# Kernel optimization log

Measured on AMD Instinct MI355X. Metric: run time of the kernel, lower is better.

The kernel has to match this reference:

```python
import jax, jax.numpy as jnp
import numpy as np

B, S, H = 8, 2048, 1024

def setup_inputs() -> dict:
    key = jax.random.key(0)
    k1, k2, k3, k4, k5, k6 = jax.random.split(key, 6)
    scale = 1.0 / np.sqrt(H)
    return {
        "hidden_states": jax.random.normal(k1, (B, S, H), dtype=jnp.float32),
        "key_padding_mask": jax.random.bernoulli(k2, 0.1, (B, S)),  # True = padded key
        "Wq_w": jax.random.normal(k3, (H, H), dtype=jnp.float32) * scale,
        "Wq_b": jax.random.normal(k4, (H,), dtype=jnp.float32) * 0.01,
        "Wk_w": jax.random.normal(k5, (H, H), dtype=jnp.float32) * scale,
        "Wk_b": jax.random.normal(k6, (H,), dtype=jnp.float32) * 0.01,
    }

def reference(hidden_states, key_padding_mask, Wq_w, Wq_b, Wk_w, Wk_b):
    # torch nn.Linear: y = x @ W.T + b
    q = jnp.einsum("bsh,oh->bso", hidden_states, Wq_w) + Wq_b
    k = jnp.einsum("bsh,oh->bso", hidden_states, Wk_w) + Wk_b
    d = q.shape[-1]
    scores = jnp.einsum("bqd,bkd->bqk", q, k) / jnp.sqrt(jnp.asarray(d, q.dtype))
    # scores[mask] -= inf  -> masked key columns become -inf
    scores = jnp.where(key_padding_mask[:, None, :], -jnp.inf, scores)
    attn = jax.nn.softmax(scores, axis=2)  # [B, S, S]
    out = jnp.einsum("bqk,bkd->bqd", attn, hidden_states)  # values = hidden_states (no proj)
    return out
```

## Files before the change

### kernel.cpp

```cpp
#include <hip/hip_runtime.h>
#include <hip/hip_bf16.h>

using bf16 = __hip_bfloat16;

using frag_ab = __attribute__((ext_vector_type(8))) short;
using frag_cd = __attribute__((ext_vector_type(4))) float;

#define TM 128
#define TN 128
#define TK 32

__device__ __forceinline__ unsigned short f2bu(float f) {
    bf16 h = __float2bfloat16(f);
    return *(unsigned short*)&h;
}
__device__ __forceinline__ float bu2f(unsigned short u) {
    unsigned int w = (unsigned int)u << 16;
    return *(float*)&w;
}

__device__ __forceinline__ void st_c(float* p, float v) { *p = v; }
__device__ __forceinline__ void st_c(bf16* p, float v)  { *p = __float2bfloat16(v); }

__device__ __forceinline__ void load16(const bf16* g, bf16* l) {
    __builtin_amdgcn_global_load_lds(
        (const __attribute__((address_space(1))) unsigned int*)g,
        (__attribute__((address_space(3))) unsigned int*)l,
        16, 0, 0);
}

template <typename TC, bool HAS_BIAS, bool MASK>
__global__ __launch_bounds__(512, 2)
void gemm8p(const bf16* __restrict__ A, const bf16* __restrict__ B,
            const float* __restrict__ bias, const int* __restrict__ mask,
            TC* __restrict__ C, int K, int lda, int ldb, int ldc,
            long sA, long sB, long sC, long sM, long sBias, float scale)
{
    __shared__ short lds[65536];

    const int bz = blockIdx.z;
    const bf16* Ab = A + (long)bz * sA;
    const bf16* Bb = B + (long)bz * sB;
    TC* Cb = C + (long)bz * sC;
    const int* maskb = MASK ? (mask + (long)bz * sM) : nullptr;
    const float* biasb = HAS_BIAS ? (bias + (long)bz * sBias) : nullptr;

    const int t    = threadIdx.x;
    const int wid  = t >> 6;
    const int lane = t & 63;
    const int m0 = blockIdx.x * 256;
    const int n0 = blockIdx.y * 256;
    const int wr = wid >> 2;
    const int wc = wid & 3;
    const int lrow = lane & 15;
    const int quad = lane >> 4;

    const int rco   = ((quad + ((lrow >> 1) & 3)) & 3) * 8;
    const int a_off = wr * 4096 + lrow * 32 + rco;
    const int b_off = wc * 2048 + lrow * 32 + rco;

    const int srow = wid * 32 + (lane >> 2);
    const int gk   = (((lane & 3) - (lane >> 3)) & 3) * 8;
    const bf16* srcA0 = Ab + (long)(m0 + srow) * lda + gk;
    const bf16* srcA1 = Ab + (long)(m0 + srow + 16) * lda + gk;
    const bf16* srcB0 = Bb + (long)(n0 + srow) * ldb + gk;
    const bf16* srcB1 = Bb + (long)(n0 + srow + 16) * ldb + gk;
    const int dst0 = wid * 1024 + lane * 8;

    frag_cd acc[8][4] = {};
    frag_ab A0[4], A1[4], B0[4], B1[4];

#define STG(SLOT, PART, K0)                                                     \
    do {                                                                        \
        load16((PART ? srcB0 : srcA0) + (K0),                                   \
               (bf16*)&lds[(SLOT) * 16384 + (PART) * 8192 + dst0]);             \
        load16((PART ? srcB1 : srcA1) + (K0),                                   \
               (bf16*)&lds[(SLOT) * 16384 + (PART) * 8192 + dst0 + 512]);       \
    } while (0)

#define LOADA(DST, SLOT, QM)                                                    \
    do {                                                                        \
        _Pragma("unroll")                                                       \
        for (int i_ = 0; i_ < 4; ++i_)                                          \
            DST[i_] = *(const frag_ab*)&lds[(SLOT) * 16384 + a_off +            \
                                            (QM) * 2048 + i_ * 512];            \
    } while (0)

#define LOADB(DST, SLOT)                                                        \
    do {                                                                        \
        _Pragma("unroll")                                                       \
        for (int j_ = 0; j_ < 4; ++j_)                                          \
            DST[j_] = *(const frag_ab*)&lds[(SLOT) * 16384 + 8192 + b_off +     \
                                            j_ * 512];                          \
    } while (0)

#define MFMA16(AR, BR, QM)                                                      \
    do {                                                                        \
        _Pragma("unroll")                                                       \
        for (int i_ = 0; i_ < 4; ++i_)                                          \
            _Pragma("unroll")                                                   \
            for (int j_ = 0; j_ < 4; ++j_)                                      \
                acc[(QM) * 4 + i_][j_] = __builtin_amdgcn_mfma_f32_16x16x32_bf16( \
                    AR[i_], BR[j_], acc[(QM) * 4 + i_][j_], 0, 0, 0);           \
    } while (0)

#define VMW(N)                                                                  \
    do {                                                                        \
        if ((N) == 6)      asm volatile("s_waitcnt vmcnt(6)" ::: "memory");     \
        else if ((N) == 4) asm volatile("s_waitcnt vmcnt(4)" ::: "memory");     \
        else if ((N) == 0) asm volatile("s_waitcnt vmcnt(0)" ::: "memory");     \
    } while (0)

#define PH(AR, BR, QM, ISSUE, NSLOT, NAR, NBR, NQM, DO_STG, SSLOT, SPART, SK0, VMN) \
    do {                                                                        \
        if ((ISSUE) >= 1) LOADA(NAR, NSLOT, NQM);                               \
        if ((ISSUE) == 2) LOADB(NBR, NSLOT);                                    \
        if (DO_STG) STG(SSLOT, SPART, SK0);                                     \
        asm volatile("" ::: "memory");                                          \
        __builtin_amdgcn_s_setprio(1);                                          \
        MFMA16(AR, BR, QM);                                                     \
        __builtin_amdgcn_s_setprio(0);                                          \
        VMW(VMN);                                                               \
        asm volatile("" ::: "memory");                                          \
        __builtin_amdgcn_s_barrier();                                           \
        asm volatile("" ::: "memory");                                          \
    } while (0)

    STG(0, 0, 0);  STG(0, 1, 0);
    STG(1, 0, 32); STG(1, 1, 32);
    STG(2, 0, 64); STG(2, 1, 64);
    asm volatile("s_waitcnt vmcnt(8)" ::: "memory");
    __builtin_amdgcn_s_barrier();
    asm volatile("" ::: "memory");
    LOADA(A0, 0, 0);
    LOADB(B0, 0);

    const int NI = K >> 7;
    for (int it = 0; it < NI - 1; ++it) {
        const int kb = it << 7;
        PH(A0, B0, 0, 1, 0, A1, B1, 1, 1, 3, 0, kb + 96,   6);
        PH(A1, B0, 1, 2, 1, A0, B1, 0, 1, 3, 1, kb + 96,  -1);
        PH(A0, B1, 0, 1, 1, A1, B0, 1, 1, 0, 0, kb + 128,  6);
        PH(A1, B1, 1, 2, 2, A0, B0, 0, 1, 0, 1, kb + 128, -1);
        PH(A0, B0, 0, 1, 2, A1, B1, 1, 1, 1, 0, kb + 160,  6);
        PH(A1, B0, 1, 2, 3, A0, B1, 0, 1, 1, 1, kb + 160, -1);
        PH(A0, B1, 0, 1, 3, A1, B0, 1, 1, 2, 0, kb + 192,  6);
        PH(A1, B1, 1, 2, 0, A0, B0, 0, 1, 2, 1, kb + 192, -1);
    }
    {
        const int kb = (NI - 1) << 7;
        PH(A0, B0, 0, 1, 0, A1, B1, 1, 1, 3, 0, kb + 96,   6);
        PH(A1, B0, 1, 2, 1, A0, B1, 0, 1, 3, 1, kb + 96,  -1);
        PH(A0, B1, 0, 1, 1, A1, B0, 1, 0, 0, 0, 0,         4);
        PH(A1, B1, 1, 2, 2, A0, B0, 0, 0, 0, 0, 0,        -1);
        PH(A0, B0, 0, 1, 2, A1, B1, 1, 0, 0, 0, 0,         0);
        PH(A1, B0, 1, 2, 3, A0, B1, 0, 0, 0, 0, 0,        -1);
        PH(A0, B1, 0, 1, 3, A1, B0, 1, 0, 0, 0, 0,        -1);
        PH(A1, B1, 1, 0, 0, A0, B0, 0, 0, 0, 0, 0,        -1);
    }
#undef PH
#undef VMW
#undef MFMA16
#undef LOADB
#undef LOADA
#undef STG

#pragma unroll
    for (int j = 0; j < 4; ++j) {
        const int col = n0 + wc * 64 + j * 16 + lrow;
        const float bv = HAS_BIAS ? biasb[col] : 0.0f;
        const bool msk = MASK ? (maskb[col] != 0) : false;
#pragma unroll
        for (int ai = 0; ai < 8; ++ai) {
            const int rbase = m0 + wr * 128 + ai * 16 + quad * 4;
#pragma unroll
            for (int r = 0; r < 4; ++r) {
                float v = acc[ai][j][r] * scale + bv;
                if (MASK && msk) v = -INFINITY;
                st_c(&Cb[(long)(rbase + r) * ldc + col], v);
            }
        }
    }
}

template <typename TC, bool HAS_BIAS, bool MASK>
__global__ __launch_bounds__(256, 4)
void mfma_gemm_nt(const bf16* __restrict__ A, const bf16* __restrict__ B,
                  const float* __restrict__ bias, const int* __restrict__ mask,
                  TC* __restrict__ C, int N, int K, int lda, int ldb, int ldc,
                  long sA, long sB, long sC, long sM, float scale)
{
    __shared__ bf16 As[2][TM][TK];
    __shared__ bf16 Bs[2][TN][TK];

    const int bz = blockIdx.z;
    const bf16* Ab = A + (long)bz * sA;
    const bf16* Bb = B + (long)bz * sB;
    TC* Cb = C + (long)bz * sC;
    const int* maskb = MASK ? (mask + (long)bz * sM) : nullptr;

    const int t  = threadIdx.x;
    const int m0 = blockIdx.x * TM;
    const int n0 = blockIdx.y * TN;

    const int srow = t >> 2;
    const int c    = t & 3;
    const int gco  = (((c - (srow >> 1)) & 3) << 3);
    const int lco  = c << 3;
    const bf16* ga0 = Ab + (long)(m0 + srow) * lda + gco;
    const bf16* ga1 = ga0 + (long)64 * lda;
    const bf16* gb0 = Bb + (long)(n0 + srow) * ldb + gco;
    const bf16* gb1 = gb0 + (long)64 * ldb;

    const int wave = t >> 6;
    const int lane = t & 63;
    const int wm   = (wave & 1) * 64;
    const int wn   = (wave >> 1) * 64;
    const int lrow = lane & 15;
    const int quad = lane >> 4;
    const int rco  = (((quad + (lrow >> 1)) & 3) << 3);

    frag_cd acc[4][4] = {};

#define STAGE(buf)                                         \
    do {                                                   \
        load16(ga0, &As[buf][srow][lco]);                  \
        load16(ga1, &As[buf][srow + 64][lco]);             \
        load16(gb0, &Bs[buf][srow][lco]);                  \
        load16(gb1, &Bs[buf][srow + 64][lco]);             \
        ga0 += TK; ga1 += TK; gb0 += TK; gb1 += TK;        \
    } while (0)

    STAGE(0);
    __syncthreads();

    int cur = 0;
    for (int k0 = 0; k0 < K; k0 += TK) {
        if (k0 + TK < K) STAGE(cur ^ 1);

        frag_ab af[4], bfv[4];
#pragma unroll
        for (int i = 0; i < 4; ++i)
            af[i] = *(const frag_ab*)&As[cur][wm + i * 16 + lrow][rco];
#pragma unroll
        for (int j = 0; j < 4; ++j)
            bfv[j] = *(const frag_ab*)&Bs[cur][wn + j * 16 + lrow][rco];
#pragma unroll
        for (int i = 0; i < 4; ++i)
#pragma unroll
            for (int j = 0; j < 4; ++j)
                acc[i][j] = __builtin_amdgcn_mfma_f32_16x16x32_bf16(
                    af[i], bfv[j], acc[i][j], 0, 0, 0);

        __syncthreads();
        cur ^= 1;
    }
#undef STAGE

#pragma unroll
    for (int j = 0; j < 4; ++j) {
        const int col = n0 + wn + j * 16 + lrow;
        const float bv = HAS_BIAS ? bias[col] : 0.0f;
        const bool msk = MASK ? (maskb[col] != 0) : false;
#pragma unroll
        for (int i = 0; i < 4; ++i) {
            const int rbase = m0 + wm + i * 16 + quad * 4;
#pragma unroll
            for (int r = 0; r < 4; ++r) {
                float v = acc[i][j][r] * scale + bv;
                if (MASK && msk) v = -INFINITY;
                st_c(&Cb[(long)(rbase + r) * ldc + col], v);
            }
        }
    }
}

__global__ __launch_bounds__(256)
void convert_transpose(const float* __restrict__ X, bf16* __restrict__ Xb,
                       bf16* __restrict__ XT, int S, int H)
{
    __shared__ unsigned short tile[64][72];
    const int b = blockIdx.z;
    const float* Xp = X + (long)b * S * H;
    bf16* Xbp = Xb + (long)b * S * H;
    bf16* XTp = XT + (long)b * H * S;
    const int h0 = blockIdx.x * 64, s0 = blockIdx.y * 64;
    const int t = threadIdx.x;
    const int r  = t >> 4;
    const int c4 = (t & 15) * 4;

#pragma unroll
    for (int p = 0; p < 4; ++p) {
        const int row = r + p * 16;
        const float4 v = *(const float4*)&Xp[(long)(s0 + row) * H + h0 + c4];
        ushort4 u;
        u.x = f2bu(v.x); u.y = f2bu(v.y); u.z = f2bu(v.z); u.w = f2bu(v.w);
        *(ushort4*)&tile[row][c4] = u;
        *(ushort4*)&Xbp[(long)(s0 + row) * H + h0 + c4] = u;
    }
    __syncthreads();
#pragma unroll
    for (int p = 0; p < 4; ++p) {
        const int hrow = r + p * 16;
        ushort4 u;
        u.x = tile[c4 + 0][hrow];
        u.y = tile[c4 + 1][hrow];
        u.z = tile[c4 + 2][hrow];
        u.w = tile[c4 + 3][hrow];
        *(ushort4*)&XTp[(long)(h0 + hrow) * S + s0 + c4] = u;
    }
}

__global__ __launch_bounds__(256)
void rowdot1024(const bf16* __restrict__ A, const float* __restrict__ x,
                float* __restrict__ y, float scale)
{
    const int wid  = threadIdx.x >> 6;
    const int lane = threadIdx.x & 63;
    const long row = (long)blockIdx.x * 4 + wid;
    const bf16* a = A + row * 1024 + lane * 16;
    const float* xp = x + lane * 16;

    frag_ab u0 = *(const frag_ab*)a;
    frag_ab u1 = *(const frag_ab*)(a + 8);
    float s = 0.0f;
#pragma unroll
    for (int i = 0; i < 8; ++i) s += bu2f((unsigned short)u0[i]) * xp[i];
#pragma unroll
    for (int i = 0; i < 8; ++i) s += bu2f((unsigned short)u1[i]) * xp[i + 8];
#pragma unroll
    for (int o = 32; o > 0; o >>= 1) s += __shfl_xor(s, o, 64);
    if (lane == 0) y[row] = s * scale;
}

__global__ __launch_bounds__(256)
void softmax_kernel(bf16* __restrict__ Smat, int Slen)
{
    const int row = blockIdx.x;
    bf16* srow = Smat + (long)row * Slen;

    const int t    = threadIdx.x;
    const int lane = t & 63;
    const int wid  = t >> 6;

    ushort4 u0 = ((const ushort4*)srow)[t * 2];
    ushort4 u1 = ((const ushort4*)srow)[t * 2 + 1];

    float vals[8];
    {
        const unsigned short us[8] = {u0.x, u0.y, u0.z, u0.w, u1.x, u1.y, u1.z, u1.w};
#pragma unroll
        for (int i = 0; i < 8; ++i) vals[i] = bu2f(us[i]);
    }

    float mx = vals[0];
#pragma unroll
    for (int i = 1; i < 8; ++i) mx = fmaxf(mx, vals[i]);

    __shared__ float red[4];
#pragma unroll
    for (int o = 32; o > 0; o >>= 1) mx = fmaxf(mx, __shfl_xor(mx, o, 64));
    if (lane == 0) red[wid] = mx;
    __syncthreads();
    mx = fmaxf(fmaxf(red[0], red[1]), fmaxf(red[2], red[3]));
    __syncthreads();

    float sum = 0.0f;
#pragma unroll
    for (int i = 0; i < 8; ++i) {
        const float e = __expf(vals[i] - mx);
        vals[i] = e;
        sum += e;
    }
#pragma unroll
    for (int o = 32; o > 0; o >>= 1) sum += __shfl_xor(sum, o, 64);
    if (lane == 0) red[wid] = sum;
    __syncthreads();
    sum = red[0] + red[1] + red[2] + red[3];

    const float inv = 1.0f / sum;
    ushort4 o0, o1;
    o0.x = f2bu(vals[0] * inv); o0.y = f2bu(vals[1] * inv);
    o0.z = f2bu(vals[2] * inv); o0.w = f2bu(vals[3] * inv);
    o1.x = f2bu(vals[4] * inv); o1.y = f2bu(vals[5] * inv);
    o1.z = f2bu(vals[6] * inv); o1.w = f2bu(vals[7] * inv);
    ((ushort4*)srow)[t * 2]     = o0;
    ((ushort4*)srow)[t * 2 + 1] = o1;
}

extern "C" void kernel_launch(void* const* d_in, const int* in_sizes, int n_in,
                              void* d_out, int out_size, void* d_ws, size_t ws_size,
                              hipStream_t stream)
{
    const float* hidden = (const float*)d_in[0];
    const int*   mask   = (const int*)d_in[1];
    const float* Wq_w   = (const float*)d_in[2];
    const float* Wq_b   = (const float*)d_in[3];
    const float* Wk_w   = (const float*)d_in[4];
    const float* Wk_b   = (const float*)d_in[5];
    float* out = (float*)d_out;

    const int B = 8, S = 2048, H = 1024;
    const int M = B * S;
    const long MH = (long)M * H;

    bf16* T   = (bf16*)d_ws;
    bf16* XbT = T + MH;
    bf16* Xb  = XbT + MH;
    bf16* Sb  = Xb + MH;
    bf16* WqT   = Sb;
    bf16* WkT   = WqT + (long)H * H;
    bf16* W2T   = WkT + (long)H * H;
    bf16* dummy = W2T + (long)H * H;
    float* wv   = (float*)(dummy + (long)H * H);
    float* vbuf = (float*)d_out;

    const dim3 blk(256);
    const dim3 blk512(512);

    convert_transpose<<<dim3(H / 64, S / 64, B), blk, 0, stream>>>(hidden, Xb, XbT, S, H);
    convert_transpose<<<dim3(H / 64, H / 64, 1), blk, 0, stream>>>(Wq_w, dummy, WqT, H, H);
    convert_transpose<<<dim3(H / 64, H / 64, 1), blk, 0, stream>>>(Wk_w, dummy, WkT, H, H);

    rowdot1024<<<dim3(H / 4), blk, 0, stream>>>(WkT, Wq_b, wv, 1.0f);
    rowdot1024<<<dim3(M / 4), blk, 0, stream>>>(Xb, wv, vbuf, 1.0f / 32.0f);

    mfma_gemm_nt<bf16, false, false><<<dim3(H / TM, H / TN, 1), blk, 0, stream>>>(
        WkT, WqT, nullptr, nullptr, W2T, H, H, H, H, H, 0, 0, 0, 0, 1.0f);

    gemm8p<bf16, false, false><<<dim3(M / 256, H / 256, 1), blk512, 0, stream>>>(
        Xb, W2T, nullptr, nullptr, T, H, H, H, H, 0, 0, 0, 0, 0, 1.0f);

    gemm8p<bf16, true, true><<<dim3(S / 256, S / 256, B), blk512, 0, stream>>>(
        T, Xb, vbuf, mask, Sb, H, H, H, S,
        (long)S * H, (long)S * H, (long)S * S, S, S, 1.0f / 32.0f);

    softmax_kernel<<<dim3(B * S), blk, 0, stream>>>(Sb, S);

    gemm8p<float, false, false><<<dim3(S / 256, H / 256, B), blk512, 0, stream>>>(
        Sb, XbT, nullptr, nullptr, out, S, S, S, H,
        (long)S * S, (long)H * S, (long)S * H, 0, 0, 1.0f);
}
```

Before: 386.2 us.

## Fuse softmax into score and PV GEMM epilogues, remap blocks across XCDs

Removes the separate softmax kernel. The score GEMM epilogue now writes exp(score) directly, with masked keys set to 0 and no row-max subtraction. The PV GEMM accumulates row sums of the bf16 probability fragments during its main loop, reduces them through LDS and divides in the epilogue. Both batched GEMMs also remap linear block IDs so the batch index follows the low bits, spreading each batch across XCDs. Dropping the max subtraction avoids a full read-modify-write pass over the S×S matrix, but it can overflow for large logits. The row-sum work also adds VALU load to one column of waves.

```diff
diff --git a/kernel.cpp b/kernel.cpp
--- a/kernel.cpp
+++ b/kernel.cpp
@@ -29,7 +29,7 @@
         16, 0, 0);
 }
 
-template <typename TC, bool HAS_BIAS, bool MASK>
+template <typename TC, bool HAS_BIAS, bool MASK, bool EXPOUT, bool ROWDIV, bool XCDZ>
 __global__ __launch_bounds__(512, 2)
 void gemm8p(const bf16* __restrict__ A, const bf16* __restrict__ B,
             const float* __restrict__ bias, const int* __restrict__ mask,
@@ -38,7 +38,15 @@
 {
     __shared__ short lds[65536];
 
-    const int bz = blockIdx.z;
+    int bx = blockIdx.x, by = blockIdx.y, bz = blockIdx.z;
+    if constexpr (XCDZ) {
+        const int L = bx + gridDim.x * (by + gridDim.y * bz);
+        bz = L & 7;
+        const int idx = L >> 3;
+        bx = idx % gridDim.x;
+        by = idx / gridDim.x;
+    }
+
     const bf16* Ab = A + (long)bz * sA;
     const bf16* Bb = B + (long)bz * sB;
     TC* Cb = C + (long)bz * sC;
@@ -48,8 +56,8 @@
     const int t    = threadIdx.x;
     const int wid  = t >> 6;
     const int lane = t & 63;
-    const int m0 = blockIdx.x * 256;
-    const int n0 = blockIdx.y * 256;
+    const int m0 = bx * 256;
+    const int n0 = by * 256;
     const int wr = wid >> 2;
     const int wc = wid & 3;
     const int lrow = lane & 15;
@@ -69,6 +77,7 @@
 
     frag_cd acc[8][4] = {};
     frag_ab A0[4], A1[4], B0[4], B1[4];
+    float rs[8] = {};
 
 #define STG(SLOT, PART, K0)                                                     \
     do {                                                                        \
@@ -102,6 +111,22 @@
             for (int j_ = 0; j_ < 4; ++j_)                                      \
                 acc[(QM) * 4 + i_][j_] = __builtin_amdgcn_mfma_f32_16x16x32_bf16( \
                     AR[i_], BR[j_], acc[(QM) * 4 + i_][j_], 0, 0, 0);           \
+    } while (0)
+
+#define RSUM(AR, QM)                                                            \
+    do {                                                                        \
+        if constexpr (ROWDIV) {                                                 \
+            if (wc == 0) {                                                      \
+                _Pragma("unroll")                                               \
+                for (int i_ = 0; i_ < 4; ++i_) {                                \
+                    float s_ = 0.0f;                                            \
+                    _Pragma("unroll")                                           \
+                    for (int e_ = 0; e_ < 8; ++e_)                              \
+                        s_ += bu2f((unsigned short)AR[i_][e_]);                 \
+                    rs[(QM) * 4 + i_] += s_;                                    \
+                }                                                               \
+            }                                                                   \
+        }                                                                       \
     } while (0)
 
 #define VMW(N)                                                                  \
@@ -120,6 +145,7 @@
         __builtin_amdgcn_s_setprio(1);                                          \
         MFMA16(AR, BR, QM);                                                     \
         __builtin_amdgcn_s_setprio(0);                                          \
+        RSUM(AR, QM);                                                           \
         VMW(VMN);                                                               \
         asm volatile("" ::: "memory");                                          \
         __builtin_amdgcn_s_barrier();                                           \
@@ -160,11 +186,35 @@
     }
 #undef PH
 #undef VMW
+#undef RSUM
 #undef MFMA16
 #undef LOADB
 #undef LOADA
 #undef STG
 
+    float inv_l[8][4] = {};
+    if constexpr (ROWDIV) {
+        float* lshare = (float*)lds;
+#pragma unroll
+        for (int x_ = 0; x_ < 8; ++x_) {
+            float s_ = rs[x_];
+            s_ += __shfl_xor(s_, 16, 64);
+            s_ += __shfl_xor(s_, 32, 64);
+            rs[x_] = s_;
+        }
+        if (wc == 0 && quad == 0) {
+#pragma unroll
+            for (int x_ = 0; x_ < 8; ++x_)
+                lshare[wr * 128 + (x_ >> 2) * 64 + (x_ & 3) * 16 + lrow] = rs[x_];
+        }
+        __syncthreads();
+#pragma unroll
+        for (int ai = 0; ai < 8; ++ai)
+#pragma unroll
+            for (int r = 0; r < 4; ++r)
+                inv_l[ai][r] = 1.0f / lshare[wr * 128 + ai * 16 + quad * 4 + r];
+    }
+
 #pragma unroll
     for (int j = 0; j < 4; ++j) {
         const int col = n0 + wc * 64 + j * 16 + lrow;
@@ -176,7 +226,12 @@
 #pragma unroll
             for (int r = 0; r < 4; ++r) {
                 float v = acc[ai][j][r] * scale + bv;
-                if (MASK && msk) v = -INFINITY;
+                if constexpr (EXPOUT) {
+                    v = (MASK && msk) ? 0.0f : __expf(v);
+                } else {
+                    if (MASK && msk) v = -INFINITY;
+                    if constexpr (ROWDIV) v *= inv_l[ai][r];
+                }
                 st_c(&Cb[(long)(rbase + r) * ldc + col], v);
             }
         }
@@ -333,61 +388,6 @@
     if (lane == 0) y[row] = s * scale;
 }
 
-__global__ __launch_bounds__(256)
-void softmax_kernel(bf16* __restrict__ Smat, int Slen)
-{
-    const int row = blockIdx.x;
-    bf16* srow = Smat + (long)row * Slen;
-
-    const int t    = threadIdx.x;
-    const int lane = t & 63;
-    const int wid  = t >> 6;
-
-    ushort4 u0 = ((const ushort4*)srow)[t * 2];
-    ushort4 u1 = ((const ushort4*)srow)[t * 2 + 1];
-
-    float vals[8];
-    {
-        const unsigned short us[8] = {u0.x, u0.y, u0.z, u0.w, u1.x, u1.y, u1.z, u1.w};
-#pragma unroll
-        for (int i = 0; i < 8; ++i) vals[i] = bu2f(us[i]);
-    }
-
-    float mx = vals[0];
-#pragma unroll
-    for (int i = 1; i < 8; ++i) mx = fmaxf(mx, vals[i]);
-
-    __shared__ float red[4];
-#pragma unroll
-    for (int o = 32; o > 0; o >>= 1) mx = fmaxf(mx, __shfl_xor(mx, o, 64));
-    if (lane == 0) red[wid] = mx;
-    __syncthreads();
-    mx = fmaxf(fmaxf(red[0], red[1]), fmaxf(red[2], red[3]));
-    __syncthreads();
-
-    float sum = 0.0f;
-#pragma unroll
-    for (int i = 0; i < 8; ++i) {
-        const float e = __expf(vals[i] - mx);
-        vals[i] = e;
-        sum += e;
-    }
-#pragma unroll
-    for (int o = 32; o > 0; o >>= 1) sum += __shfl_xor(sum, o, 64);
-    if (lane == 0) red[wid] = sum;
-    __syncthreads();
-    sum = red[0] + red[1] + red[2] + red[3];
-
-    const float inv = 1.0f / sum;
-    ushort4 o0, o1;
-    o0.x = f2bu(vals[0] * inv); o0.y = f2bu(vals[1] * inv);
-    o0.z = f2bu(vals[2] * inv); o0.w = f2bu(vals[3] * inv);
-    o1.x = f2bu(vals[4] * inv); o1.y = f2bu(vals[5] * inv);
-    o1.z = f2bu(vals[6] * inv); o1.w = f2bu(vals[7] * inv);
-    ((ushort4*)srow)[t * 2]     = o0;
-    ((ushort4*)srow)[t * 2 + 1] = o1;
-}
-
 extern "C" void kernel_launch(void* const* d_in, const int* in_sizes, int n_in,
                               void* d_out, int out_size, void* d_ws, size_t ws_size,
                               hipStream_t stream)
@@ -428,16 +428,17 @@
     mfma_gemm_nt<bf16, false, false><<<dim3(H / TM, H / TN, 1), blk, 0, stream>>>(
         WkT, WqT, nullptr, nullptr, W2T, H, H, H, H, H, 0, 0, 0, 0, 1.0f);
 
-    gemm8p<bf16, false, false><<<dim3(M / 256, H / 256, 1), blk512, 0, stream>>>(
+    gemm8p<bf16, false, false, false, false, false>
+        <<<dim3(M / 256, H / 256, 1), blk512, 0, stream>>>(
         Xb, W2T, nullptr, nullptr, T, H, H, H, H, 0, 0, 0, 0, 0, 1.0f);
 
-    gemm8p<bf16, true, true><<<dim3(S / 256, S / 256, B), blk512, 0, stream>>>(
+    gemm8p<bf16, true, true, true, false, true>
+        <<<dim3(S / 256, S / 256, B), blk512, 0, stream>>>(
         T, Xb, vbuf, mask, Sb, H, H, H, S,
         (long)S * H, (long)S * H, (long)S * S, S, S, 1.0f / 32.0f);
 
-    softmax_kernel<<<dim3(B * S), blk, 0, stream>>>(Sb, S);
-
-    gemm8p<float, false, false><<<dim3(S / 256, H / 256, B), blk512, 0, stream>>>(
+    gemm8p<float, false, false, false, true, true>
+        <<<dim3(S / 256, H / 256, B), blk512, 0, stream>>>(
         Sb, XbT, nullptr, nullptr, out, S, S, S, H,
         (long)S * S, (long)H * S, (long)S * H, 0, 0, 1.0f);
 }
```

Result: slower. 466.5 us (+20.8%).
